# Performance work log

Measured on AMD Instinct MI355X. Metric: run time of the kernel, lower is better.

Reference implementation:

```python
import jax, jax.numpy as jnp
import numpy as np
import math

ANCHORS = np.array([[1.3221, 1.73145, 0.0],
                    [3.19275, 4.00944, 0.3927],
                    [5.05587, 8.09892, 0.7854],
                    [9.47112, 4.84053, 1.1781],
                    [11.2364, 10.0071, 1.5708]], dtype=np.float32)
NUM_CLASSES = 80
COORD_SCALE, NOOBJ_SCALE, OBJ_SCALE, CLASS_SCALE, THETA_SCALE = 5.0, 1.0, 5.0, 1.0, 5.0
B, G, H, W = 32, 16, 64, 64
A = ANCHORS.shape[0]


def setup_inputs() -> dict:
    key = jax.random.key(0)
    k1, k2, k3, k4, k5 = jax.random.split(key, 5)
    output = jax.random.normal(k1, (B, A * (6 + NUM_CLASSES), H, W), jnp.float32)
    # unique grid cell per box within each image -> scatter indices never collide
    cells = jax.vmap(lambda k: jax.random.permutation(k, H * W)[:G])(jax.random.split(k2, B))  # [B,G]
    frac = jax.random.uniform(k3, (B, G, 2)) * 0.999
    cx = ((cells % W).astype(jnp.float32) + frac[..., 0]) / W
    cy = ((cells // W).astype(jnp.float32) + frac[..., 1]) / H
    wh = jax.random.uniform(k4, (B, G, 2), minval=0.02, maxval=0.9)
    th = jax.random.uniform(k5, (B, G), minval=0.0, maxval=8.0)
    gt_boxes = jnp.concatenate([cx[..., None], cy[..., None], wh, th[..., None]], axis=-1)
    gt_cls = jax.random.randint(jax.random.fold_in(key, 7), (B, G), 0, NUM_CLASSES)
    return {"output": output, "gt_boxes": gt_boxes, "gt_cls": gt_cls}


def build_targets(gt_boxes, gt_cls):
    aw = jnp.asarray(ANCHORS[:, 0]); ah = jnp.asarray(ANCHORS[:, 1]); aa = jnp.asarray(ANCHORS[:, 2])
    gx = gt_boxes[..., 0] * W
    gy = gt_boxes[..., 1] * H
    gw = gt_boxes[..., 2] * W
    gh = gt_boxes[..., 3] * H
    gth = gt_boxes[..., 4] * (math.pi / 8)
    # angle-based anchor matching: cos(0.25*(gt_theta - anchor_theta))  [B,G,A]
    iou = jnp.cos(0.25 * (gth[..., None] - aa))
    best = jnp.argmax(iou, axis=-1)            # [B,G]
    iou_best = jnp.max(iou, axis=-1)           # [B,G]
    gi = jnp.clip(gx.astype(jnp.int32), 0, W - 1)
    gj = jnp.clip(gy.astype(jnp.int32), 0, H - 1)
    cell = gj * W + gi                          # [B,G]
    b_idx = jnp.broadcast_to(jnp.arange(B)[:, None], (B, G))
    tx = gx - gi
    ty = gy - gj
    tw = jnp.log(jnp.maximum(gw, 1.0) / aw[best])
    th_ = jnp.log(jnp.maximum(gh, 1.0) / ah[best])
    tth = gth - aa[best]
    HW = H * W
    conf_mask = jnp.full((B, A, HW), NOOBJ_SCALE, jnp.float32).at[b_idx, best, cell].set(OBJ_SCALE)
    obj_mask = jnp.zeros((B, A, HW), bool).at[b_idx, best, cell].set(True)
    tcoord = jnp.zeros((B, A, 4, HW), jnp.float32)
    for k, v in enumerate((tx, ty, tw, th_)):
        tcoord = tcoord.at[b_idx, best, k, cell].set(v)
    tconf = jnp.zeros((B, A, HW), jnp.float32).at[b_idx, best, cell].set(iou_best)
    ttheta = jnp.zeros((B, A, HW), jnp.float32).at[b_idx, best, cell].set(tth)
    tcls = jnp.zeros((B, A, HW), jnp.int32).at[b_idx, best, cell].set(gt_cls.astype(jnp.int32))
    return obj_mask, conf_mask, tcoord, tconf, tcls, ttheta


def reference(output, gt_boxes, gt_cls):
    HW = H * W
    out = output.reshape(B, A, 6 + NUM_CLASSES, HW)
    coord = jnp.concatenate([jax.nn.sigmoid(out[:, :, :2]), out[:, :, 2:4]], axis=2)  # [B,A,4,HW]
    conf = jax.nn.sigmoid(out[:, :, 4])          # [B,A,HW]
    theta = out[:, :, 5]                          # [B,A,HW]
    cls_logits = out[:, :, 6:].transpose(0, 1, 3, 2)  # [B,A,HW,C]
    obj_mask, conf_mask, tcoord, tconf, tcls, ttheta = build_targets(gt_boxes, gt_cls)
    cm = obj_mask[:, :, None, :].astype(coord.dtype)
    # MSELoss(mean over ALL elements) of masked tensors, as in the torch code
    loss_coord = COORD_SCALE * jnp.mean(((coord - tcoord) * cm) ** 2)
    loss_conf = jnp.mean(((conf - tconf) * conf_mask) ** 2)
    mf = obj_mask.astype(coord.dtype)
    n = jnp.sum(mf)
    # CrossEntropyLoss(mean) over boolean-masked cells == weighted mean
    logp = jax.nn.log_softmax(cls_logits, axis=-1)
    nll = -jnp.take_along_axis(logp, tcls[..., None], axis=-1)[..., 0]  # [B,A,HW]
    loss_cls = CLASS_SCALE * 2.0 * jnp.sum(nll * mf) / n
    # SmoothL1Loss(mean, beta=1) over masked cells
    d = jnp.abs(theta - ttheta)
    sl = jnp.where(d < 1.0, 0.5 * d * d, d - 0.5)
    loss_theta = THETA_SCALE * jnp.sum(sl * mf) / n
    loss_tot = loss_coord + loss_conf + loss_cls + loss_theta
    return (loss_tot, loss_coord, loss_conf, loss_cls, loss_theta)
```

## Files before the change

### kernel.cpp

```cpp
#include <hip/hip_runtime.h>
#include <math.h>

#define Bn 32
#define Gn 16
#define Hn 64
#define Wn 64
#define An 5
#define NCn 80
#define HWn 4096
#define CHn 86
#define CHBn (An * CHn)

__device__ __constant__ float d_aw[5] = {1.3221f, 3.19275f, 5.05587f, 9.47112f, 11.2364f};
__device__ __constant__ float d_ah[5] = {1.73145f, 4.00944f, 8.09892f, 4.84053f, 10.0071f};
__device__ __constant__ float d_aa[5] = {0.0f, 0.3927f, 0.7854f, 1.1781f, 1.5708f};

__device__ __forceinline__ float sigmoidf_(float x) {
    return 1.0f / (1.0f + expf(-x));
}

__global__ void yolo_main(const float* __restrict__ outp,
                          const float* __restrict__ gtb,
                          const int* __restrict__ gtc,
                          float* __restrict__ ws) {
    const int bid = blockIdx.x;
    if (bid < 640) {
        int t = bid * 256 + threadIdx.x;
        int hw4 = t & 1023;
        int ra  = t >> 10;
        int a   = ra % 5;
        int b   = ra / 5;
        const float4* p = (const float4*)(outp + (size_t)(b * CHBn + a * CHn + 4) * HWn);
        float4 v = p[hw4];
        float s0 = sigmoidf_(v.x);
        float s1 = sigmoidf_(v.y);
        float s2 = sigmoidf_(v.z);
        float s3 = sigmoidf_(v.w);
        float local = s0 * s0 + s1 * s1 + s2 * s2 + s3 * s3;
        #pragma unroll
        for (int off = 32; off > 0; off >>= 1)
            local += __shfl_down(local, off, 64);
        __shared__ float smem[4];
        int lane = threadIdx.x & 63;
        int wv   = threadIdx.x >> 6;
        if (lane == 0) smem[wv] = local;
        __syncthreads();
        if (threadIdx.x == 0)
            atomicAdd(&ws[1], smem[0] + smem[1] + smem[2] + smem[3]);
    } else {
        int j = (bid - 640) * 256 + threadIdx.x;
        int b = j >> 4;
        int g = j & 15;
        const float* gt = gtb + (size_t)(b * Gn + g) * 5;
        float gx  = gt[0] * Wn;
        float gy  = gt[1] * Hn;
        float gw  = gt[2] * Wn;
        float gh  = gt[3] * Hn;
        float gth = gt[4] * 0.39269908169872414f;

        float best_iou = -1e30f;
        int best = 0;
        #pragma unroll
        for (int a = 0; a < 5; a++) {
            float iou = cosf(0.25f * (gth - d_aa[a]));
            if (iou > best_iou) { best_iou = iou; best = a; }
        }

        int gi = (int)gx; gi = gi < 0 ? 0 : (gi > Wn - 1 ? Wn - 1 : gi);
        int gj = (int)gy; gj = gj < 0 ? 0 : (gj > Hn - 1 ? Hn - 1 : gj);
        int cell = gj * Wn + gi;

        float tx  = gx - (float)gi;
        float ty  = gy - (float)gj;
        float tw  = logf(fmaxf(gw, 1.0f) / d_aw[best]);
        float th_ = logf(fmaxf(gh, 1.0f) / d_ah[best]);
        float tth = gth - d_aa[best];

        const float* base = outp + (size_t)(b * CHBn + best * CHn) * HWn + cell;
        float c0  = base[0];
        float c1  = base[HWn];
        float c2  = base[2 * HWn];
        float c3  = base[3 * HWn];
        float cf  = base[4 * HWn];
        float thv = base[5 * HWn];

        float p0 = sigmoidf_(c0);
        float p1 = sigmoidf_(c1);
        float d0 = p0 - tx, d1 = p1 - ty, d2 = c2 - tw, d3 = c3 - th_;
        float coord = d0 * d0 + d1 * d1 + d2 * d2 + d3 * d3;

        float s  = sigmoidf_(cf);
        float dc = 5.0f * (s - best_iou);
        float confcorr = dc * dc - s * s;

        float dth = fabsf(thv - tth);
        float sl  = dth < 1.0f ? 0.5f * dth * dth : dth - 0.5f;

        float lg[80];
        #pragma unroll
        for (int c = 0; c < 80; c++) lg[c] = base[(6 + c) * HWn];
        float m = -1e30f;
        #pragma unroll
        for (int c = 0; c < 80; c++) m = fmaxf(m, lg[c]);
        float se = 0.0f;
        #pragma unroll
        for (int c = 0; c < 80; c++) se += expf(lg[c] - m);
        float lse = logf(se) + m;
        int tc = gtc[b * Gn + g];
        float nll = lse - lg[tc];

        atomicAdd(&ws[0], coord);
        atomicAdd(&ws[1], confcorr);
        atomicAdd(&ws[2], nll);
        atomicAdd(&ws[3], sl);
    }
}

__global__ void yolo_final(const float* __restrict__ ws, float* __restrict__ out5) {
    float coord = 5.0f * ws[0] / 2621440.0f;
    float conf  = ws[1] / 655360.0f;
    float cls   = 2.0f * ws[2] / 512.0f;
    float th    = 5.0f * ws[3] / 512.0f;
    out5[0] = coord + conf + cls + th;
    out5[1] = coord;
    out5[2] = conf;
    out5[3] = cls;
    out5[4] = th;
}

extern "C" void kernel_launch(void* const* d_in, const int* in_sizes, int n_in,
                              void* d_out, int out_size, void* d_ws, size_t ws_size,
                              hipStream_t stream) {
    const float* outp = (const float*)d_in[0];
    const float* gtb  = (const float*)d_in[1];
    const int*   gtc  = (const int*)d_in[2];
    float* out5 = (float*)d_out;
    float* ws   = (float*)d_ws;

    hipMemsetAsync(ws, 0, 4 * sizeof(float), stream);
    yolo_main<<<642, 256, 0, stream>>>(outp, gtb, gtc, ws);
    yolo_final<<<1, 1, 0, stream>>>(ws, out5);
}
```

Before: 322.0 us.

## Use wavefront-per-box class softmax and per-block slots instead of atomics

Measured after the change: 257.7 us. -20.0%, faster.

```diff
diff --git a/kernel.cpp b/kernel.cpp
--- a/kernel.cpp
+++ b/kernel.cpp
@@ -11,6 +11,10 @@
 #define CHn 86
 #define CHBn (An * CHn)
 
+#define NCONF_BLK 160
+#define NGT_BLK   128
+#define NBLK      (NCONF_BLK + NGT_BLK)
+
 __device__ __constant__ float d_aw[5] = {1.3221f, 3.19275f, 5.05587f, 9.47112f, 11.2364f};
 __device__ __constant__ float d_ah[5] = {1.73145f, 4.00944f, 8.09892f, 4.84053f, 10.0071f};
 __device__ __constant__ float d_aa[5] = {0.0f, 0.3927f, 0.7854f, 1.1781f, 1.5708f};
@@ -19,36 +23,39 @@
     return 1.0f / (1.0f + expf(-x));
 }
 
-__global__ void yolo_main(const float* __restrict__ outp,
-                          const float* __restrict__ gtb,
-                          const int* __restrict__ gtc,
-                          float* __restrict__ ws) {
-    const int bid = blockIdx.x;
-    if (bid < 640) {
-        int t = bid * 256 + threadIdx.x;
-        int hw4 = t & 1023;
-        int ra  = t >> 10;
-        int a   = ra % 5;
-        int b   = ra / 5;
+__global__ __launch_bounds__(256) void yolo_main(const float* __restrict__ outp,
+                                                 const float* __restrict__ gtb,
+                                                 const int* __restrict__ gtc,
+                                                 float4* __restrict__ slots) {
+    const int bid  = blockIdx.x;
+    const int tid  = threadIdx.x;
+    const int lane = tid & 63;
+    const int wv   = tid >> 6;
+    __shared__ float4 smem[4];
+
+    if (bid < NCONF_BLK) {
+        int a = bid % 5;
+        int b = bid / 5;
         const float4* p = (const float4*)(outp + (size_t)(b * CHBn + a * CHn + 4) * HWn);
-        float4 v = p[hw4];
-        float s0 = sigmoidf_(v.x);
-        float s1 = sigmoidf_(v.y);
-        float s2 = sigmoidf_(v.z);
-        float s3 = sigmoidf_(v.w);
-        float local = s0 * s0 + s1 * s1 + s2 * s2 + s3 * s3;
+        float local = 0.0f;
         #pragma unroll
-        for (int off = 32; off > 0; off >>= 1)
-            local += __shfl_down(local, off, 64);
-        __shared__ float smem[4];
-        int lane = threadIdx.x & 63;
-        int wv   = threadIdx.x >> 6;
-        if (lane == 0) smem[wv] = local;
+        for (int k = 0; k < 4; k++) {
+            float4 v = p[tid + 256 * k];
+            float s0 = sigmoidf_(v.x), s1 = sigmoidf_(v.y);
+            float s2 = sigmoidf_(v.z), s3 = sigmoidf_(v.w);
+            local += s0 * s0 + s1 * s1 + s2 * s2 + s3 * s3;
+        }
+        #pragma unroll
+        for (int m = 32; m > 0; m >>= 1)
+            local += __shfl_xor(local, m, 64);
+        if (lane == 0) smem[wv] = make_float4(0.f, local, 0.f, 0.f);
         __syncthreads();
-        if (threadIdx.x == 0)
-            atomicAdd(&ws[1], smem[0] + smem[1] + smem[2] + smem[3]);
+        if (tid == 0) {
+            float c = smem[0].y + smem[1].y + smem[2].y + smem[3].y;
+            slots[bid] = make_float4(0.f, c, 0.f, 0.f);
+        }
     } else {
-        int j = (bid - 640) * 256 + threadIdx.x;
+        int j = (bid - NCONF_BLK) * 4 + wv;
         int b = j >> 4;
         int g = j & 15;
         const float* gt = gtb + (size_t)(b * Gn + g) * 5;
@@ -77,12 +84,28 @@
         float tth = gth - d_aa[best];
 
         const float* base = outp + (size_t)(b * CHBn + best * CHn) * HWn + cell;
-        float c0  = base[0];
-        float c1  = base[HWn];
-        float c2  = base[2 * HWn];
-        float c3  = base[3 * HWn];
-        float cf  = base[4 * HWn];
-        float thv = base[5 * HWn];
+
+        float lg0 = base[(6 + lane) * HWn];
+        float lg1 = (lane < 16) ? base[(6 + 64 + lane) * HWn] : -1e30f;
+        float hv = (lane < 6) ? base[lane * HWn] : 0.0f;
+
+        float m = fmaxf(lg0, lg1);
+        #pragma unroll
+        for (int s = 32; s > 0; s >>= 1)
+            m = fmaxf(m, __shfl_xor(m, s, 64));
+        float e = expf(lg0 - m) + ((lane < 16) ? expf(lg1 - m) : 0.0f);
+        #pragma unroll
+        for (int s = 32; s > 0; s >>= 1)
+            e += __shfl_xor(e, s, 64);
+        float lse = logf(e) + m;
+
+        int tc = gtc[b * Gn + g];
+        float ltc = (tc < 64) ? __shfl(lg0, tc, 64) : __shfl(lg1, tc - 64, 64);
+        float nll = lse - ltc;
+
+        float c0 = __shfl(hv, 0, 64), c1 = __shfl(hv, 1, 64);
+        float c2 = __shfl(hv, 2, 64), c3 = __shfl(hv, 3, 64);
+        float cf = __shfl(hv, 4, 64), thv = __shfl(hv, 5, 64);
 
         float p0 = sigmoidf_(c0);
         float p1 = sigmoidf_(c1);
@@ -96,36 +119,56 @@
         float dth = fabsf(thv - tth);
         float sl  = dth < 1.0f ? 0.5f * dth * dth : dth - 0.5f;
 
-        float lg[80];
-        #pragma unroll
-        for (int c = 0; c < 80; c++) lg[c] = base[(6 + c) * HWn];
-        float m = -1e30f;
-        #pragma unroll
-        for (int c = 0; c < 80; c++) m = fmaxf(m, lg[c]);
-        float se = 0.0f;
-        #pragma unroll
-        for (int c = 0; c < 80; c++) se += expf(lg[c] - m);
-        float lse = logf(se) + m;
-        int tc = gtc[b * Gn + g];
-        float nll = lse - lg[tc];
-
-        atomicAdd(&ws[0], coord);
-        atomicAdd(&ws[1], confcorr);
-        atomicAdd(&ws[2], nll);
-        atomicAdd(&ws[3], sl);
+        if (lane == 0) smem[wv] = make_float4(coord, confcorr, nll, sl);
+        __syncthreads();
+        if (tid == 0) {
+            float4 r = smem[0];
+            float4 q1 = smem[1], q2 = smem[2], q3 = smem[3];
+            r.x += q1.x + q2.x + q3.x;
+            r.y += q1.y + q2.y + q3.y;
+            r.z += q1.z + q2.z + q3.z;
+            r.w += q1.w + q2.w + q3.w;
+            slots[bid] = r;
+        }
     }
 }
 
-__global__ void yolo_final(const float* __restrict__ ws, float* __restrict__ out5) {
-    float coord = 5.0f * ws[0] / 2621440.0f;
-    float conf  = ws[1] / 655360.0f;
-    float cls   = 2.0f * ws[2] / 512.0f;
-    float th    = 5.0f * ws[3] / 512.0f;
-    out5[0] = coord + conf + cls + th;
-    out5[1] = coord;
-    out5[2] = conf;
-    out5[3] = cls;
-    out5[4] = th;
+__global__ __launch_bounds__(256) void yolo_final(const float4* __restrict__ slots,
+                                                  float* __restrict__ out5) {
+    const int tid  = threadIdx.x;
+    const int lane = tid & 63;
+    const int wv   = tid >> 6;
+    float4 acc = make_float4(0.f, 0.f, 0.f, 0.f);
+    for (int i = tid; i < NBLK; i += 256) {
+        float4 v = slots[i];
+        acc.x += v.x; acc.y += v.y; acc.z += v.z; acc.w += v.w;
+    }
+    #pragma unroll
+    for (int s = 32; s > 0; s >>= 1) {
+        acc.x += __shfl_xor(acc.x, s, 64);
+        acc.y += __shfl_xor(acc.y, s, 64);
+        acc.z += __shfl_xor(acc.z, s, 64);
+        acc.w += __shfl_xor(acc.w, s, 64);
+    }
+    __shared__ float4 smem[4];
+    if (lane == 0) smem[wv] = acc;
+    __syncthreads();
+    if (tid == 0) {
+        float4 r = smem[0];
+        r.x += smem[1].x + smem[2].x + smem[3].x;
+        r.y += smem[1].y + smem[2].y + smem[3].y;
+        r.z += smem[1].z + smem[2].z + smem[3].z;
+        r.w += smem[1].w + smem[2].w + smem[3].w;
+        float coord = 5.0f * r.x / 2621440.0f;
+        float conf  = r.y / 655360.0f;
+        float cls   = 2.0f * r.z / 512.0f;
+        float th    = 5.0f * r.w / 512.0f;
+        out5[0] = coord + conf + cls + th;
+        out5[1] = coord;
+        out5[2] = conf;
+        out5[3] = cls;
+        out5[4] = th;
+    }
 }
 
 extern "C" void kernel_launch(void* const* d_in, const int* in_sizes, int n_in,
@@ -134,10 +177,9 @@
     const float* outp = (const float*)d_in[0];
     const float* gtb  = (const float*)d_in[1];
     const int*   gtc  = (const int*)d_in[2];
-    float* out5 = (float*)d_out;
-    float* ws   = (float*)d_ws;
+    float* out5  = (float*)d_out;
+    float4* slots = (float4*)d_ws;
 
-    hipMemsetAsync(ws, 0, 4 * sizeof(float), stream);
-    yolo_main<<<642, 256, 0, stream>>>(outp, gtb, gtc, ws);
-    yolo_final<<<1, 1, 0, stream>>>(ws, out5);
+    yolo_main<<<NBLK, 256, 0, stream>>>(outp, gtb, gtc, slots);
+    yolo_final<<<1, 256, 0, stream>>>(slots, out5);
 }
```
